# Performance work log

Hardware: AMD Instinct MI355X
Metric: run time of the kernel (lower is better)

Reference implementation:

```python
import jax, jax.numpy as jnp
import numpy as np
from jax import lax

NMS_TOPN = 300
IOU_THR = 0.5
TOTAL_LABELS = 21
TOTAL_POS = 64
TOTAL_NEG = 64
POOL_H, POOL_W = 7, 7
NEG_INF = jnp.float32(-1e9)


def decode_boxes(anchors, deltas):
    # anchors/deltas: (B, N, 4) in (y1, x1, y2, x2) / (dy, dx, dh, dw)
    aw = anchors[..., 3] - anchors[..., 1]
    ah = anchors[..., 2] - anchors[..., 0]
    acx = anchors[..., 1] + 0.5 * aw
    acy = anchors[..., 0] + 0.5 * ah
    w = jnp.exp(deltas[..., 3]) * aw
    h = jnp.exp(deltas[..., 2]) * ah
    cx = deltas[..., 1] * aw + acx
    cy = deltas[..., 0] * ah + acy
    y1 = cy - 0.5 * h
    x1 = cx - 0.5 * w
    return jnp.stack([y1, x1, y1 + h, x1 + w], axis=-1)


def pairwise_iou(b1, b2):
    # b1 (N,4), b2 (M,4) -> (N,M)
    yt = jnp.maximum(b1[:, None, 0], b2[None, :, 0])
    xt = jnp.maximum(b1[:, None, 1], b2[None, :, 1])
    yb = jnp.minimum(b1[:, None, 2], b2[None, :, 2])
    xb = jnp.minimum(b1[:, None, 3], b2[None, :, 3])
    inter = jnp.maximum(yb - yt, 0.0) * jnp.maximum(xb - xt, 0.0)
    a1 = (b1[:, 2] - b1[:, 0]) * (b1[:, 3] - b1[:, 1])
    a2 = (b2[:, 2] - b2[:, 0]) * (b2[:, 3] - b2[:, 1])
    union = a1[:, None] + a2[None, :] - inter
    return jnp.where(union > 0, inter / union, 0.0)


def nms_single(boxes, scores):
    # Greedy NMS equivalent to tf.image.combined_non_max_suppression with 1 class,
    # iou_threshold=0.5, score_threshold=-inf, clip_boxes=True, padded to NMS_TOPN.
    def step(sc, _):
        idx = jnp.argmax(sc)
        valid = sc[idx] > NEG_INF * 0.5
        iou = pairwise_iou(boxes[idx][None, :], boxes)[0]
        sc = jnp.where(iou > IOU_THR, NEG_INF, sc)
        sc = sc.at[idx].set(NEG_INF)
        return sc, (idx, valid)

    _, (idxs, valids) = lax.scan(step, scores, None, length=NMS_TOPN)
    sel = jnp.clip(boxes[idxs], 0.0, 1.0)
    return jnp.where(valids[:, None], sel, 0.0)


def get_deltas_from_bboxes(bboxes, gt_boxes):
    bw = bboxes[..., 3] - bboxes[..., 1]
    bh = bboxes[..., 2] - bboxes[..., 0]
    bcx = bboxes[..., 1] + 0.5 * bw
    bcy = bboxes[..., 0] + 0.5 * bh
    gw = gt_boxes[..., 3] - gt_boxes[..., 1]
    gh = gt_boxes[..., 2] - gt_boxes[..., 0]
    gcx = gt_boxes[..., 1] + 0.5 * gw
    gcy = gt_boxes[..., 0] + 0.5 * gh
    bw = jnp.where(bw == 0, 1e-3, bw)
    bh = jnp.where(bh == 0, 1e-3, bh)
    dx = jnp.where(gw == 0, 0.0, (gcx - bcx) / bw)
    dy = jnp.where(gh == 0, 0.0, (gcy - bcy) / bh)
    dw = jnp.where(gw == 0, 0.0, jnp.log(jnp.maximum(gw, 1e-12) / bw))
    dh = jnp.where(gh == 0, 0.0, jnp.log(jnp.maximum(gh, 1e-12) / bh))
    return jnp.stack([dy, dx, dh, dw], axis=-1)


def crop_and_resize(image, boxes, box_indices, ph, pw):
    # Faithful tf.image.crop_and_resize (bilinear, extrapolation_value=0).
    B, H, W, C = image.shape
    y1, x1, y2, x2 = boxes[:, 0], boxes[:, 1], boxes[:, 2], boxes[:, 3]
    iy = jnp.arange(ph, dtype=image.dtype) / (ph - 1)
    ix = jnp.arange(pw, dtype=image.dtype) / (pw - 1)
    ys = y1[:, None] * (H - 1) + iy[None, :] * ((y2 - y1)[:, None] * (H - 1))  # (R, ph)
    xs = x1[:, None] * (W - 1) + ix[None, :] * ((x2 - x1)[:, None] * (W - 1))  # (R, pw)
    y0 = jnp.floor(ys)
    x0 = jnp.floor(xs)
    wy = ys - y0
    wx = xs - x0
    y0i = jnp.clip(y0.astype(jnp.int32), 0, H - 1)
    y1i = jnp.clip(y0i + 1, 0, H - 1)
    x0i = jnp.clip(x0.astype(jnp.int32), 0, W - 1)
    x1i = jnp.clip(x0i + 1, 0, W - 1)
    b = box_indices[:, None, None]

    def g(yi, xi):  # -> (R, ph, pw, C)
        return image[b, yi[:, :, None], xi[:, None, :], :]

    wxs = wx[:, None, :, None]
    top = g(y0i, x0i) * (1 - wxs) + g(y0i, x1i) * wxs
    bot = g(y1i, x0i) * (1 - wxs) + g(y1i, x1i) * wxs
    out = top * (1 - wy)[:, :, None, None] + bot * wy[:, :, None, None]
    valid = ((ys >= 0) & (ys <= H - 1))[:, :, None] & ((xs >= 0) & (xs <= W - 1))[:, None, :]
    return jnp.where(valid[..., None], out, 0.0)


def _forward(feature_map, rpn_bbox_deltas, rpn_labels, anchors, gt_boxes, gt_labels):
    B, H, W, C = feature_map.shape
    total_bboxes = TOTAL_POS + TOTAL_NEG

    rpn_bboxes = decode_boxes(anchors, rpn_bbox_deltas)            # (B, N, 4)
    nms_bboxes = jax.vmap(nms_single)(rpn_bboxes, rpn_labels)      # (B, topn, 4)

    def select_single(boxes, gt):  # helpers.get_selected_indices
        iou = pairwise_iou(boxes, gt)                              # (topn, M)
        merged = iou.max(axis=1)
        max_gt = jnp.argmax(iou, axis=1).astype(jnp.int32)
        order = jnp.argsort(-merged)
        pos = order[:TOTAL_POS]
        neg = order[TOTAL_POS:TOTAL_POS + TOTAL_NEG]
        return jnp.concatenate([pos, neg]).astype(jnp.int32), max_gt[pos]

    bbox_indices, gt_box_indices = jax.vmap(select_single)(nms_bboxes, gt_boxes)
    roi_bboxes = jnp.take_along_axis(nms_bboxes, bbox_indices[..., None], axis=1)
    roi_bboxes = lax.stop_gradient(roi_bboxes)                     # (B, T, 4)

    pooling_bboxes = roi_bboxes.reshape(B * total_bboxes, 4)
    pooling_idx = jnp.repeat(jnp.arange(B, dtype=jnp.int32), total_bboxes)
    pooled = crop_and_resize(feature_map, pooling_bboxes, pooling_idx, POOL_H, POOL_W)
    final_pool = pooled.reshape(B, total_bboxes, POOL_H, POOL_W, C)

    pos_gt_boxes = jnp.take_along_axis(gt_boxes, gt_box_indices[..., None], axis=1)
    gt_boxes_map = jnp.concatenate(
        [pos_gt_boxes, jnp.zeros((B, TOTAL_NEG, 4), feature_map.dtype)], axis=1)
    pos_gt_labels = jnp.take_along_axis(gt_labels, gt_box_indices, axis=1)
    gt_labels_map = jnp.concatenate(
        [pos_gt_labels, jnp.full((B, TOTAL_NEG), TOTAL_LABELS - 1, gt_labels.dtype)], axis=1)

    roi_deltas = get_deltas_from_bboxes(roi_bboxes, gt_boxes_map)  # (B, T, 4)
    # scatter_nd into (B, T, L, 4) with unique (b, box, label) indices == one-hot expand
    onehot = jax.nn.one_hot(gt_labels_map, TOTAL_LABELS, dtype=roi_deltas.dtype)
    roi_bbox_deltas = (onehot[..., None] * roi_deltas[:, :, None, :]).reshape(
        B, total_bboxes, TOTAL_LABELS * 4)
    roi_bbox_labels = jax.nn.one_hot(gt_labels_map, TOTAL_LABELS, dtype=jnp.int32)
    return (final_pool,
            lax.stop_gradient(roi_bbox_deltas),
            lax.stop_gradient(roi_bbox_labels))


def _rand_boxes(key, lead_shape):
    k1, k2 = jax.random.split(key)
    cyx = jax.random.uniform(k1, lead_shape + (2,), minval=0.1, maxval=0.9)
    hw = jax.random.uniform(k2, lead_shape + (2,), minval=0.05, maxval=0.3)
    y1x1 = jnp.clip(cyx - 0.5 * hw, 0.0, 1.0)
    y2x2 = jnp.clip(cyx + 0.5 * hw, 0.0, 1.0)
    return jnp.concatenate([y1x1[..., 0:1], y1x1[..., 1:2], y2x2[..., 0:1], y2x2[..., 1:2]], axis=-1)


def setup_inputs() -> dict:
    key = jax.random.key(0)
    ks = jax.random.split(key, 6)
    B, N, M, H, W, C = 4, 36864, 16, 64, 64, 512
    feature_map = jax.random.normal(ks[0], (B, H, W, C), jnp.float32)
    rpn_bbox_deltas = 0.1 * jax.random.normal(ks[1], (B, N, 4), jnp.float32)
    rpn_labels = jax.random.uniform(ks[2], (B, N), dtype=jnp.float32)  # objectness scores
    anchors = _rand_boxes(ks[3], (B, N))
    gt_boxes = _rand_boxes(ks[4], (B, M))
    gt_labels = jax.random.randint(ks[5], (B, M), 0, 20).astype(jnp.int32)
    return {"feature_map": feature_map, "rpn_bbox_deltas": rpn_bbox_deltas,
            "rpn_labels": rpn_labels, "anchors": anchors,
            "gt_boxes": gt_boxes, "gt_labels": gt_labels}


def reference(feature_map, rpn_bbox_deltas, rpn_labels, anchors, gt_boxes, gt_labels):
    return _forward(feature_map, rpn_bbox_deltas, rpn_labels, anchors, gt_boxes, gt_labels)
```

## Files before the change

### kernel.cpp

```cpp
#include <hip/hip_runtime.h>
#include <math.h>

#define BATCH      4
#define N_RPN      36864
#define NMS_TOPN   300
#define IOU_THR    0.5f
#define TOTAL_LABELS 21
#define TOTAL_POS  64
#define TOTAL_BOX  128
#define GT_M       16
#define FM_H       64
#define FM_W       64
#define FM_C       512
#define POOL_H     7
#define POOL_W     7
#define MCAP       4096
#define MWORDS     (MCAP / 64)
#define NBUCK      1024
#define JCHUNKS    16

typedef unsigned long long u64;

#define OUT_POOL_ELEMS   ((size_t)BATCH * TOTAL_BOX * POOL_H * POOL_W * FM_C)
#define OUT_DELTA_ELEMS  ((size_t)BATCH * TOTAL_BOX * TOTAL_LABELS * 4)

__global__ __launch_bounds__(1024) void compact_kernel(
    const float* __restrict__ scores, u64* __restrict__ keysG,
    int* __restrict__ mCounts)
{
    const int b = blockIdx.x;
    const int t = threadIdx.x;
    const int lane = t & 63;
    const int wave = t >> 6;
    __shared__ unsigned hist[NBUCK];
    __shared__ unsigned s_suf[NBUCK];
    __shared__ unsigned s_wincl[16];
    __shared__ int s_cnt, s_thresh;

    hist[t] = 0u;
    if (t == 0) { s_cnt = 0; s_thresh = NBUCK - 1; }
    __syncthreads();

    const float* sc = scores + (size_t)b * N_RPN;
    for (int i = t; i < N_RPN; i += 1024) {
        int bk = (int)(sc[i] * 1024.0f);
        bk = min(max(bk, 0), NBUCK - 1);
        atomicAdd(&hist[bk], 1u);
    }
    __syncthreads();

    unsigned v = hist[t];
    #pragma unroll
    for (int off = 1; off < 64; off <<= 1) {
        unsigned o = __shfl_down(v, off, 64);
        if (lane + off < 64) v += o;
    }
    if (lane == 0) s_wincl[wave] = v;
    __syncthreads();
    if (wave == 0 && lane < 16) {
        unsigned wv = s_wincl[lane];
        #pragma unroll
        for (int off = 1; off < 16; off <<= 1) {
            unsigned o = __shfl_down(wv, off, 64);
            if (lane + off < 16) wv += o;
        }
        s_wincl[lane] = wv;
    }
    __syncthreads();
    unsigned suf = v + ((wave < 15) ? s_wincl[wave + 1] : 0u);
    s_suf[t] = suf;
    __syncthreads();
    if (suf <= MCAP && (t == 0 || s_suf[t - 1] > MCAP)) s_thresh = t;
    __syncthreads();
    const int thresh = s_thresh;

    u64* kg = keysG + (size_t)b * MCAP;
    for (int i = t; i < N_RPN; i += 1024) {
        float s = sc[i];
        int bk = min(max((int)(s * 1024.0f), 0), NBUCK - 1);
        if (bk >= thresh) {
            int p = atomicAdd(&s_cnt, 1);
            kg[p] = ((u64)__float_as_uint(s) << 32) | (unsigned)(~(unsigned)i);
        }
    }
    __syncthreads();
    const int M = s_cnt;
    for (int p = M + t; p < MCAP; p += 1024) kg[p] = 0ULL;
    if (t == 0) mCounts[b] = M;
}

__global__ __launch_bounds__(256) void rank_partial_kernel(
    const u64* __restrict__ keysG, int* __restrict__ partial)
{
    const int b  = blockIdx.z;
    const int jc = blockIdx.y;
    const int ic = blockIdx.x;
    const int t  = threadIdx.x;
    __shared__ u64 s_j[256];
    const u64* kg = keysG + (size_t)b * MCAP;
    s_j[t] = kg[jc * 256 + t];
    __syncthreads();

    const int i = ic * 256 + t;
    const u64 ki = kg[i];
    const int jbase = jc * 256;
    int cnt = 0;
    const ulonglong2* k2 = (const ulonglong2*)s_j;
    #pragma unroll 8
    for (int j2 = 0; j2 < 128; ++j2) {
        ulonglong2 kk = k2[j2];
        int j = jbase + j2 * 2;
        cnt += (kk.x > ki) || (kk.x == ki && j < i);
        cnt += (kk.y > ki) || (kk.y == ki && (j + 1) < i);
    }
    partial[((size_t)b * JCHUNKS + jc) * MCAP + i] = cnt;
}

__global__ __launch_bounds__(256) void rank_finalize_kernel(
    const u64* __restrict__ keysG, const float* __restrict__ anchors,
    const float* __restrict__ deltas, const int* __restrict__ mCounts,
    const int* __restrict__ partial, float4* __restrict__ sortedBoxes)
{
    const int b = blockIdx.y;
    const int t = threadIdx.x;
    const int i = blockIdx.x * 256 + t;

    int rank = 0;
    #pragma unroll
    for (int jc = 0; jc < JCHUNKS; ++jc)
        rank += partial[((size_t)b * JCHUNKS + jc) * MCAP + i];

    const u64 ki = keysG[(size_t)b * MCAP + i];
    const int M = mCounts[b];
    float4 o = make_float4(0.f, 0.f, 0.f, 0.f);
    if (i < M) {
        unsigned idx = ~(unsigned)(ki & 0xFFFFFFFFULL);
        const float* a = anchors + ((size_t)b * N_RPN + idx) * 4;
        const float* d = deltas  + ((size_t)b * N_RPN + idx) * 4;
        float aw  = a[3] - a[1];
        float ah  = a[2] - a[0];
        float acx = a[1] + 0.5f * aw;
        float acy = a[0] + 0.5f * ah;
        float ww  = expf(d[3]) * aw;
        float hh  = expf(d[2]) * ah;
        float cx  = d[1] * aw + acx;
        float cy  = d[0] * ah + acy;
        float y1  = cy - 0.5f * hh;
        float x1  = cx - 0.5f * ww;
        o = make_float4(y1, x1, y1 + hh, x1 + ww);
    }
    sortedBoxes[(size_t)b * MCAP + rank] = o;
}

__global__ __launch_bounds__(256) void nms_mask_kernel(
    const float4* __restrict__ sortedBoxes, u64* __restrict__ mask)
{
    const int b  = blockIdx.z;
    const int r0 = blockIdx.x * 64;
    const int c0 = blockIdx.y * 256;
    u64* mk = mask + (size_t)b * (MWORDS * MCAP);
    const int t  = threadIdx.x;
    const int lr = t & 63;
    const int wq = t >> 6;
    const int r  = r0 + lr;
    const int w  = (c0 >> 6) + wq;

    if (c0 + 255 <= r0) {
        mk[(size_t)w * MCAP + r] = 0ULL;
        return;
    }
    __shared__ float4 s_c[256];
    const float4* sb = sortedBoxes + (size_t)b * MCAP;
    s_c[t] = sb[c0 + t];
    float4 bi = sb[r];
    __syncthreads();

    float ai = (bi.z - bi.x) * (bi.w - bi.y);
    u64 bits = 0ULL;
    const int jb = w * 64;
    if (jb + 63 > r) {
        for (int k = 0; k < 64; ++k) {
            float4 bj = s_c[wq * 64 + k];
            float yt = fmaxf(bi.x, bj.x);
            float xt = fmaxf(bi.y, bj.y);
            float yb = fminf(bi.z, bj.z);
            float xb = fminf(bi.w, bj.w);
            float inter = fmaxf(yb - yt, 0.f) * fmaxf(xb - xt, 0.f);
            float aj = (bj.z - bj.x) * (bj.w - bj.y);
            float un = ai + aj - inter;
            bool sup = (jb + k > r) && (un > 0.f) && ((inter / un) > IOU_THR);
            bits |= ((u64)sup) << k;
        }
    }
    mk[(size_t)w * MCAP + r] = bits;
}

__global__ __launch_bounds__(64) void nms_scan_kernel(
    const float4* __restrict__ sortedBoxes, const int* __restrict__ mCounts,
    const u64* __restrict__ mask, float4* __restrict__ selBoxes)
{
    const int b = blockIdx.x;
    const int l = threadIdx.x;
    const u64* mkl = mask + (size_t)b * (MWORDS * MCAP) + (size_t)l * MCAP;
    __shared__ int s_sel[NMS_TOPN];
    const int M = mCounts[b];
    const int lo = l * 64;
    u64 bound = (lo + 64 <= M) ? ~0ULL
              : ((lo >= M) ? 0ULL : ((1ULL << (M - lo)) - 1ULL));
    u64 sup = 0ULL;
    int cnt = 0;

    while (cnt < NMS_TOPN) {
        u64 avw = ~sup & bound;
        int idx[16];
        #pragma unroll
        for (int m = 0; m < 16; ++m) {
            u64 bal = __ballot(avw != 0ULL);
            if (bal == 0ULL) { idx[m] = -1; continue; }
            int L = __ffsll((long long)bal) - 1;
            unsigned wl = (unsigned)__shfl((int)(unsigned)avw, L, 64);
            unsigned wh = (unsigned)__shfl((int)(unsigned)(avw >> 32), L, 64);
            u64 aw = ((u64)wh << 32) | (u64)wl;
            int bit = __ffsll((long long)aw) - 1;
            idx[m] = L * 64 + bit;
            if (l == L) avw &= ~(1ULL << bit);
        }
        if (idx[0] < 0) break;

        u64 rows[16];
        #pragma unroll
        for (int m = 0; m < 16; ++m)
            rows[m] = (idx[m] >= 0) ? mkl[idx[m]] : 0ULL;

        u64 acc = 0ULL;
        #pragma unroll
        for (int m = 0; m < 16; ++m) {
            int im = idx[m];
            if (im < 0 || cnt >= NMS_TOPN) break;
            int Lm = im >> 6, bm = im & 63;
            u64 kb = __ballot((l == Lm) && ((acc >> bm) & 1ULL));
            if (kb == 0ULL) {
                if (l == 0) s_sel[cnt] = im;
                cnt++;
                acc |= rows[m];
                if (l == Lm) acc |= (1ULL << bm);
            }
        }
        sup |= acc;
    }
    __syncthreads();

    for (int r = l; r < NMS_TOPN; r += 64) {
        float4 o = make_float4(0.f, 0.f, 0.f, 0.f);
        if (r < cnt) {
            float4 bx = sortedBoxes[(size_t)b * MCAP + s_sel[r]];
            o.x = fminf(fmaxf(bx.x, 0.f), 1.f);
            o.y = fminf(fmaxf(bx.y, 0.f), 1.f);
            o.z = fminf(fmaxf(bx.z, 0.f), 1.f);
            o.w = fminf(fmaxf(bx.w, 0.f), 1.f);
        }
        selBoxes[(size_t)b * NMS_TOPN + r] = o;
    }
}

__global__ __launch_bounds__(512) void select_kernel(
    const float4* __restrict__ selBoxes, const float* __restrict__ gt_boxes,
    const int* __restrict__ gt_labels, float4* __restrict__ roiBoxes,
    float4* __restrict__ gtMap, int* __restrict__ labMap)
{
    const int b = blockIdx.x;
    const int t = threadIdx.x;
    __shared__ float4 sb[NMS_TOPN];
    __shared__ float4 gt[GT_M];
    __shared__ float  merged[NMS_TOPN];
    __shared__ int    mgt[NMS_TOPN];
    __shared__ short  order[TOTAL_BOX];

    if (t < NMS_TOPN) sb[t] = selBoxes[(size_t)b * NMS_TOPN + t];
    if (t < GT_M) gt[t] = ((const float4*)gt_boxes)[b * GT_M + t];
    __syncthreads();

    if (t < NMS_TOPN) {
        float4 bx = sb[t];
        float a1 = (bx.z - bx.x) * (bx.w - bx.y);
        float best = -1.f; int arg = 0;
        for (int j = 0; j < GT_M; ++j) {
            float4 g = gt[j];
            float yt = fmaxf(bx.x, g.x), xt = fmaxf(bx.y, g.y);
            float yb = fminf(bx.z, g.z), xb = fminf(bx.w, g.w);
            float inter = fmaxf(yb - yt, 0.f) * fmaxf(xb - xt, 0.f);
            float a2 = (g.z - g.x) * (g.w - g.y);
            float un = a1 + a2 - inter;
            float iou = (un > 0.f) ? (inter / un) : 0.f;
            if (iou > best) { best = iou; arg = j; }
        }
        merged[t] = best; mgt[t] = arg;
    }
    __syncthreads();

    if (t < NMS_TOPN) {
        float mi = merged[t];
        int rank = 0;
        for (int j = 0; j < NMS_TOPN; ++j) {
            float mj = merged[j];
            rank += (mj > mi) || (mj == mi && j < t);
        }
        if (rank < TOTAL_BOX) order[rank] = (short)t;
    }
    __syncthreads();

    if (t < TOTAL_BOX) {
        int i = order[t];
        roiBoxes[(size_t)b * TOTAL_BOX + t] = sb[i];
        float4 g = make_float4(0.f, 0.f, 0.f, 0.f);
        int lab = TOTAL_LABELS - 1;
        if (t < TOTAL_POS) {
            int gi = mgt[i];
            g = gt[gi];
            lab = gt_labels[b * GT_M + gi];
        }
        gtMap[(size_t)b * TOTAL_BOX + t] = g;
        labMap[b * TOTAL_BOX + t] = lab;
    }
}

__global__ __launch_bounds__(256) void pool_kernel(
    const float* __restrict__ fm, const float4* __restrict__ roiBoxes,
    float* __restrict__ out)
{
    const int b  = blockIdx.y;
    const int r  = blockIdx.x / POOL_H;
    const int py = blockIdx.x % POOL_H;
    const int t  = threadIdx.x;

    float4 bx = roiBoxes[(size_t)b * TOTAL_BOX + r];
    float y1 = bx.x, x1 = bx.y, y2 = bx.z, x2 = bx.w;

    float iy = (float)py / 6.0f;
    float cy = (y2 - y1) * 63.0f;
    float ys = y1 * 63.0f + iy * cy;
    float fy0 = floorf(ys);
    float wy = ys - fy0;
    int y0i = min(max((int)fy0, 0), FM_H - 1);
    int y1i = min(y0i + 1, FM_H - 1);
    bool vy = (ys >= 0.f) && (ys <= 63.f);

    float cx = (x2 - x1) * 63.0f;
    const float2* f2 = (const float2*)fm;
    float2* o2 = (float2*)out;
    size_t obase = ((((size_t)b * TOTAL_BOX + r) * POOL_H + py) * POOL_W) * 256 + t;
    size_t brow = (size_t)b * FM_H;

    for (int px = 0; px < POOL_W; ++px) {
        float ix = (float)px / 6.0f;
        float xs = x1 * 63.0f + ix * cx;
        float fx0 = floorf(xs);
        float wx = xs - fx0;
        int x0i = min(max((int)fx0, 0), FM_W - 1);
        int x1i = min(x0i + 1, FM_W - 1);
        bool vx = (xs >= 0.f) && (xs <= 63.f);

        float2 g00 = f2[((brow + y0i) * FM_W + x0i) * 256 + t];
        float2 g01 = f2[((brow + y0i) * FM_W + x1i) * 256 + t];
        float2 g10 = f2[((brow + y1i) * FM_W + x0i) * 256 + t];
        float2 g11 = f2[((brow + y1i) * FM_W + x1i) * 256 + t];

        float tx = 1.f - wx, ty = 1.f - wy;
        float top0 = g00.x * tx + g01.x * wx;
        float top1 = g00.y * tx + g01.y * wx;
        float bot0 = g10.x * tx + g11.x * wx;
        float bot1 = g10.y * tx + g11.y * wx;
        float o0 = top0 * ty + bot0 * wy;
        float o1 = top1 * ty + bot1 * wy;
        if (!(vy && vx)) { o0 = 0.f; o1 = 0.f; }
        o2[obase + (size_t)px * 256] = make_float2(o0, o1);
    }
}

__global__ __launch_bounds__(256) void finalize_kernel(
    const float4* __restrict__ roiBoxes, const float4* __restrict__ gtMap,
    const int* __restrict__ labMap, float* __restrict__ out_deltas,
    float* __restrict__ out_labels)
{
    int tid = blockIdx.x * blockDim.x + threadIdx.x;
    if (tid >= BATCH * TOTAL_BOX) return;
    float4 bb = roiBoxes[tid];
    float4 g  = gtMap[tid];
    int lab   = labMap[tid];

    float bw = bb.w - bb.y, bh = bb.z - bb.x;
    float bcx = bb.y + 0.5f * bw, bcy = bb.x + 0.5f * bh;
    float gw = g.w - g.y, gh = g.z - g.x;
    float gcx = g.y + 0.5f * gw, gcy = g.x + 0.5f * gh;
    float bw2 = (bw == 0.f) ? 0.001f : bw;
    float bh2 = (bh == 0.f) ? 0.001f : bh;
    float dx = (gw == 0.f) ? 0.f : (gcx - bcx) / bw2;
    float dy = (gh == 0.f) ? 0.f : (gcy - bcy) / bh2;
    float dw = (gw == 0.f) ? 0.f : logf(fmaxf(gw, 1e-12f) / bw2);
    float dh = (gh == 0.f) ? 0.f : logf(fmaxf(gh, 1e-12f) / bh2);
    float dlt[4] = {dy, dx, dh, dw};

    float* od = out_deltas + (size_t)tid * (TOTAL_LABELS * 4);
    for (int k = 0; k < TOTAL_LABELS * 4; ++k)
        od[k] = ((k >> 2) == lab) ? dlt[k & 3] : 0.f;
    float* ol = out_labels + (size_t)tid * TOTAL_LABELS;
    for (int c = 0; c < TOTAL_LABELS; ++c)
        ol[c] = (c == lab) ? 1.0f : 0.0f;
}

extern "C" void kernel_launch(void* const* d_in, const int* in_sizes, int n_in,
                              void* d_out, int out_size, void* d_ws, size_t ws_size,
                              hipStream_t stream) {
    (void)in_sizes; (void)n_in; (void)out_size; (void)ws_size;
    const float* fm         = (const float*)d_in[0];
    const float* rpn_deltas = (const float*)d_in[1];
    const float* rpn_scores = (const float*)d_in[2];
    const float* anchors    = (const float*)d_in[3];
    const float* gt_boxes   = (const float*)d_in[4];
    const int*   gt_labels  = (const int*)d_in[5];
    float* out = (float*)d_out;

    char* w = (char*)d_ws;
    size_t off = 0;
    auto take = [&](size_t bytes) -> char* {
        char* p = w + off;
        off = (off + bytes + 255) & ~(size_t)255;
        return p;
    };
    float4* sortedBoxes = (float4*)take((size_t)BATCH * MCAP * 16);
    u64*    keysG       = (u64*)take((size_t)BATCH * MCAP * 8);
    int*    mCounts     = (int*)take(BATCH * sizeof(int));
    int*    partial     = (int*)take((size_t)BATCH * JCHUNKS * MCAP * 4);
    float4* selBoxes    = (float4*)take((size_t)BATCH * NMS_TOPN * 16);
    float4* roiBoxes    = (float4*)take((size_t)BATCH * TOTAL_BOX * 16);
    float4* gtMap       = (float4*)take((size_t)BATCH * TOTAL_BOX * 16);
    int*    labMap      = (int*)take((size_t)BATCH * TOTAL_BOX * 4);
    u64*    mask        = (u64*)take((size_t)BATCH * MWORDS * MCAP * 8);

    compact_kernel<<<BATCH, 1024, 0, stream>>>(rpn_scores, keysG, mCounts);
    rank_partial_kernel<<<dim3(MCAP / 256, JCHUNKS, BATCH), 256, 0, stream>>>(
        keysG, partial);
    rank_finalize_kernel<<<dim3(MCAP / 256, BATCH), 256, 0, stream>>>(
        keysG, anchors, rpn_deltas, mCounts, partial, sortedBoxes);
    nms_mask_kernel<<<dim3(MCAP / 64, MCAP / 256, BATCH), 256, 0, stream>>>(
        sortedBoxes, mask);
    nms_scan_kernel<<<BATCH, 64, 0, stream>>>(sortedBoxes, mCounts, mask, selBoxes);
    select_kernel<<<BATCH, 512, 0, stream>>>(selBoxes, gt_boxes, gt_labels,
                                             roiBoxes, gtMap, labMap);
    pool_kernel<<<dim3(TOTAL_BOX * POOL_H, BATCH), 256, 0, stream>>>(fm, roiBoxes, out);
    finalize_kernel<<<2, 256, 0, stream>>>(roiBoxes, gtMap, labMap,
                                           out + OUT_POOL_ELEMS,
                                           out + OUT_POOL_ELEMS + OUT_DELTA_ELEMS);
}
```

Baseline: 292.3 us.

## Resolve NMS greedily per 64-box word via fixed-point kill-set iteration

The serial greedy NMS scan, which picked one candidate at a time through ballots and shuffles in batches of 16, is replaced by word-at-a-time processing. For each 64-candidate word the keep set is computed by iterating kept = available & ~OR(rows of kept) to a fixed point, using shared-memory atomics. The kept rows are then ORed into the per-lane suppression state with batched loads. This aims to cut the per-candidate serial dependency chain, but adds block barriers per iteration and up to 64 iterations for dense intra-word chains.

```diff
diff --git a/kernel.cpp b/kernel.cpp
--- a/kernel.cpp
+++ b/kernel.cpp
@@ -201,52 +201,73 @@
 {
     const int b = blockIdx.x;
     const int l = threadIdx.x;
-    const u64* mkl = mask + (size_t)b * (MWORDS * MCAP) + (size_t)l * MCAP;
+    const u64* mkb = mask + (size_t)b * (MWORDS * MCAP);
+    const u64* mkl = mkb + (size_t)l * MCAP;
     __shared__ int s_sel[NMS_TOPN];
+    __shared__ unsigned s_klo, s_khi;
     const int M = mCounts[b];
-    const int lo = l * 64;
-    u64 bound = (lo + 64 <= M) ? ~0ULL
-              : ((lo >= M) ? 0ULL : ((1ULL << (M - lo)) - 1ULL));
     u64 sup = 0ULL;
     int cnt = 0;
 
-    while (cnt < NMS_TOPN) {
-        u64 avw = ~sup & bound;
-        int idx[16];
-        #pragma unroll
-        for (int m = 0; m < 16; ++m) {
-            u64 bal = __ballot(avw != 0ULL);
-            if (bal == 0ULL) { idx[m] = -1; continue; }
-            int L = __ffsll((long long)bal) - 1;
-            unsigned wl = (unsigned)__shfl((int)(unsigned)avw, L, 64);
-            unsigned wh = (unsigned)__shfl((int)(unsigned)(avw >> 32), L, 64);
-            u64 aw = ((u64)wh << 32) | (u64)wl;
-            int bit = __ffsll((long long)aw) - 1;
-            idx[m] = L * 64 + bit;
-            if (l == L) avw &= ~(1ULL << bit);
-        }
-        if (idx[0] < 0) break;
-
-        u64 rows[16];
-        #pragma unroll
-        for (int m = 0; m < 16; ++m)
-            rows[m] = (idx[m] >= 0) ? mkl[idx[m]] : 0ULL;
-
-        u64 acc = 0ULL;
-        #pragma unroll
-        for (int m = 0; m < 16; ++m) {
-            int im = idx[m];
-            if (im < 0 || cnt >= NMS_TOPN) break;
-            int Lm = im >> 6, bm = im & 63;
-            u64 kb = __ballot((l == Lm) && ((acc >> bm) & 1ULL));
-            if (kb == 0ULL) {
-                if (l == 0) s_sel[cnt] = im;
-                cnt++;
-                acc |= rows[m];
-                if (l == Lm) acc |= (1ULL << bm);
+    for (int k = 0; k < MWORDS; ++k) {
+        if (cnt >= NMS_TOPN) break;
+        const int lo_k = k * 64;
+        if (lo_k >= M) break;
+        const u64 bound = (lo_k + 64 <= M) ? ~0ULL
+                                           : ((1ULL << (M - lo_k)) - 1ULL);
+        unsigned blo = (unsigned)__shfl((int)(unsigned)sup, k, 64);
+        unsigned bhi = (unsigned)__shfl((int)(unsigned)(sup >> 32), k, 64);
+        const u64 avw = ~(((u64)bhi << 32) | (u64)blo) & bound;
+        if (avw == 0ULL) continue;
+
+        const u64 rw = mkb[(size_t)k * MCAP + lo_k + l];
+
+        u64 sel = avw;
+        for (int it = 0; it < 66; ++it) {
+            if (l == 0) { s_klo = 0u; s_khi = 0u; }
+            __syncthreads();
+            if ((sel >> l) & 1ULL) {
+                unsigned rl = (unsigned)rw, rh = (unsigned)(rw >> 32);
+                if (rl) atomicOr(&s_klo, rl);
+                if (rh) atomicOr(&s_khi, rh);
             }
-        }
-        sup |= acc;
+            __syncthreads();
+            u64 kill = ((u64)s_khi << 32) | (u64)s_klo;
+            u64 nsel = avw & ~kill;
+            if (nsel == sel) break;
+            sel = nsel;
+        }
+
+        const int rank_l = __popcll(sel & ((1ULL << l) - 1ULL));
+        int pc = __popcll(sel);
+        const int rem = NMS_TOPN - cnt;
+        if (pc > rem) {
+            sel = __ballot(((sel >> l) & 1ULL) && (rank_l < rem));
+            pc = rem;
+        }
+        if ((sel >> l) & 1ULL) s_sel[cnt + rank_l] = lo_k + l;
+        cnt += pc;
+
+        if (cnt < NMS_TOPN) {
+            u64 acc = 0ULL;
+            #define NMS_LD(g, m)  { const int j = (g) * 16 + (m);              \
+                const u64 rr = mkl[lo_k + j];                                  \
+                q |= (((sel >> j) & 1ULL) ? rr : 0ULL); }
+            #define NMS_GRP(g)                                                 \
+            if ((sel >> ((g) * 16)) & 0xFFFFULL) {                             \
+                u64 q = 0ULL;                                                  \
+                NMS_LD(g,0)  NMS_LD(g,1)  NMS_LD(g,2)  NMS_LD(g,3)             \
+                NMS_LD(g,4)  NMS_LD(g,5)  NMS_LD(g,6)  NMS_LD(g,7)             \
+                NMS_LD(g,8)  NMS_LD(g,9)  NMS_LD(g,10) NMS_LD(g,11)            \
+                NMS_LD(g,12) NMS_LD(g,13) NMS_LD(g,14) NMS_LD(g,15)            \
+                acc |= q;                                                      \
+            }
+            NMS_GRP(0) NMS_GRP(1) NMS_GRP(2) NMS_GRP(3)
+            #undef NMS_GRP
+            #undef NMS_LD
+            sup |= acc;
+        }
+        __syncthreads();
     }
     __syncthreads();
 
```

Result: faster. 239.8 us (-18.0%).
